# Kernel tuning notes

Hardware: AMD Instinct MI355X
Metric: run time of the kernel (lower is better)

## Reference

```python
import jax, jax.numpy as jnp
import numpy as np

N = 16384
HID = 256
MI = 128
POS_PER_NODE = 4
TEMP = 0.5


def setup_inputs() -> dict:
    key = jax.random.key(0)
    k1, k2, k3, k4 = jax.random.split(key, 4)
    h_v1 = jax.random.normal(k1, (N, HID), dtype=jnp.float32)
    h_v2 = jax.random.normal(k2, (N, HID), dtype=jnp.float32)
    W = jax.random.normal(k3, (HID, MI), dtype=jnp.float32) * (1.0 / np.sqrt(HID))
    b = jnp.zeros((MI,), dtype=jnp.float32)
    # 4 positives per row -> every row has a nonzero positive count
    pos_row = jnp.repeat(jnp.arange(N, dtype=jnp.int32), POS_PER_NODE)
    pos_col = jax.random.randint(k4, (N * POS_PER_NODE,), 0, N, dtype=jnp.int32)
    return {"h_v1": h_v1, "h_v2": h_v2, "W": W, "b": b,
            "pos_row": pos_row, "pos_col": pos_col}


def _l2norm(x):
    return x / jnp.linalg.norm(x, axis=-1, keepdims=True)


def _cal_loss_mi(e1, e2, pos_row, pos_col):
    # sim_mat[i,j] = <e1_i, e2_j> / T   (N x N, the big intermediate)
    sim = jnp.einsum('ik,jk->ij', e1, e2) / TEMP
    sim = sim - jax.lax.stop_gradient(jnp.max(sim, axis=1, keepdims=True))
    sim = jnp.exp(sim)
    sim_pos = sim[pos_row, pos_col]                      # [E] gather
    row_sum = jnp.sum(sim, axis=1)                       # [N]
    pos_sum = jax.ops.segment_sum(sim_pos, pos_row, num_segments=N)
    denom = (row_sum - pos_sum)[pos_row]                 # [E]
    log_lv = jnp.log(sim_pos / denom)                    # [E]
    pos_cnt = jax.ops.segment_sum(jnp.ones_like(sim_pos), pos_row, num_segments=N)
    per_row = jax.ops.segment_sum(log_lv, pos_row, num_segments=N) / pos_cnt
    return -jnp.mean(per_row)


def reference(h_v1, h_v2, W, b, pos_row, pos_col):
    p1 = _l2norm(jax.nn.relu(h_v1 @ W + b))
    p2 = _l2norm(jax.nn.relu(h_v2 @ W + b))
    loss = 0.5 * (_cal_loss_mi(p1, p2, pos_row, pos_col)
                  + _cal_loss_mi(p2, p1, pos_row, pos_col))
    return loss
```

## Files before the change

kernel.cpp:

```cpp
#include <hip/hip_runtime.h>

typedef unsigned short ushort_t;
typedef unsigned int uint32;
typedef __attribute__((ext_vector_type(8))) short short8;
typedef __attribute__((ext_vector_type(4))) float f32x4;
typedef __attribute__((ext_vector_type(2))) float f32x2;

#define HID 256
#define MI 128
#define ALPHA 2.8853900817779268f
#define LN2F 0.69314718055994531f

__device__ __forceinline__ float bflo(uint32 u) { return __uint_as_float(u << 16); }
__device__ __forceinline__ float bfhi(uint32 u) { return __uint_as_float(u & 0xffff0000u); }
__device__ __forceinline__ ushort_t f2bf(float f) {
  uint32 u = __float_as_uint(f);
  u += 0x7fffu + ((u >> 16) & 1u);
  return (ushort_t)(u >> 16);
}

__global__ __launch_bounds__(256) void proj_kernel(
    const float* __restrict__ h1, const float* __restrict__ h2,
    const float* __restrict__ W, const float* __restrict__ b,
    ushort_t* __restrict__ p1b, ushort_t* __restrict__ p2b,
    float* __restrict__ fbase, int nz, float* __restrict__ out, int n)
{
  __shared__ __align__(16) unsigned char wt[65536];
  int t = threadIdx.x;
  int lane = t & 63, w = t >> 6;
  int lr = lane & 15, lg = lane >> 4;
  long R0 = (long)blockIdx.x * 64;
  const float* src = (R0 < n) ? (h1 + R0 * HID) : (h2 + (R0 - n) * HID);
  ushort_t* dst = (R0 < n) ? (p1b + R0 * MI) : (p2b + (R0 - n) * MI);
  float scale = (R0 < n) ? ALPHA : 1.0f;

  {
    int base = blockIdx.x * 224;
    if (t < 224 && base + t < nz) fbase[base + t] = 0.f;
    if (blockIdx.x == 0 && t == 0) out[0] = 0.f;
  }

  #pragma unroll
  for (int i = 0; i < 32; ++i) {
    int idx4 = i * 1024 + t * 4;
    float4 v = *(const float4*)(W + idx4);
    int k = idx4 >> 7, nc0 = idx4 & 127;
    int g = k >> 3, klo = (k & 7) * 2;
    #pragma unroll
    for (int j = 0; j < 4; ++j) {
      int nc = nc0 + j;
      float f = (j == 0) ? v.x : (j == 1) ? v.y : (j == 2) ? v.z : v.w;
      *(ushort_t*)(wt + nc * 512 + ((g ^ (nc & 31)) << 4) + klo) = f2bf(f);
    }
  }

  float bb[8];
  #pragma unroll
  for (int ch = 0; ch < 8; ++ch) bb[ch] = b[ch * 16 + lr];

  int row = w * 16 + lr;
  const float* hrow = src + (size_t)row * HID;
  float4 v0[8], v1[8];
  #pragma unroll
  for (int kt = 0; kt < 8; ++kt) {
    v0[kt] = *(const float4*)(hrow + kt * 32 + lg * 8);
    v1[kt] = *(const float4*)(hrow + kt * 32 + lg * 8 + 4);
  }
  short8 afr[8];
  #pragma unroll
  for (int kt = 0; kt < 8; ++kt) {
    short8 a;
    a[0] = (short)f2bf(v0[kt].x); a[1] = (short)f2bf(v0[kt].y);
    a[2] = (short)f2bf(v0[kt].z); a[3] = (short)f2bf(v0[kt].w);
    a[4] = (short)f2bf(v1[kt].x); a[5] = (short)f2bf(v1[kt].y);
    a[6] = (short)f2bf(v1[kt].z); a[7] = (short)f2bf(v1[kt].w);
    afr[kt] = a;
  }

  __syncthreads();

  f32x4 acc[8];
  #pragma unroll
  for (int ch = 0; ch < 8; ++ch) acc[ch] = (f32x4){0.f, 0.f, 0.f, 0.f};
  #pragma unroll
  for (int ch = 0; ch < 8; ++ch) {
    int ncol = ch * 16 + lr;
    #pragma unroll
    for (int kt = 0; kt < 8; ++kt) {
      int g = kt * 4 + lg;
      short8 bf = *(const short8*)(wt + ncol * 512 + ((g ^ (ncol & 31)) << 4));
      acc[ch] = __builtin_amdgcn_mfma_f32_16x16x32_bf16(afr[kt], bf, acc[ch], 0, 0, 0);
    }
  }

  #pragma unroll
  for (int r = 0; r < 4; ++r) {
    float v[8];
    float ss = 0.f;
    #pragma unroll
    for (int ch = 0; ch < 8; ++ch) {
      v[ch] = fmaxf(acc[ch][r] + bb[ch], 0.f);
      ss += v[ch] * v[ch];
    }
    ss += __shfl_xor(ss, 1, 64);
    ss += __shfl_xor(ss, 2, 64);
    ss += __shfl_xor(ss, 4, 64);
    ss += __shfl_xor(ss, 8, 64);
    float rn = rsqrtf(ss) * scale;
    int orow = w * 16 + lg * 4 + r;
    #pragma unroll
    for (int ch = 0; ch < 8; ++ch)
      dst[(size_t)orow * MI + ch * 16 + lr] = f2bf(v[ch] * rn);
  }
}

__global__ __launch_bounds__(256, 2) void sim_kernel(
    const ushort_t* __restrict__ p1b, const ushort_t* __restrict__ p2b,
    float* __restrict__ rowsum, float* __restrict__ colsum,
    const int* __restrict__ pos_row, const int* __restrict__ pos_col,
    float* __restrict__ psum1, float* __restrict__ psum2,
    float* __restrict__ srow1, float* __restrict__ srow2,
    float* __restrict__ cntb, int E)
{
  __shared__ __align__(16) unsigned char ldsB[65536];
  __shared__ float colacc[1024];
  int t = threadIdx.x;
  int lane = t & 63, w = t >> 6;
  int lr = lane & 15, lg = lane >> 4;
  int rowbase = blockIdx.y * 256 + w * 64;
  int jbase = blockIdx.x * 1024;

  uint4 st0, st1, st2, st3;
  int gs = t & 15, r0 = t >> 4;
  int sw = (gs ^ (r0 & 15)) << 4;

  auto load_stage = [&](int jt) {
    int j0 = jbase + jt * 64;
    const ushort_t* base = p2b + (size_t)(j0 + r0) * MI + (gs << 3);
    st0 = *(const uint4*)(base);
    st1 = *(const uint4*)(base + 16 * MI);
    st2 = *(const uint4*)(base + 32 * MI);
    st3 = *(const uint4*)(base + 48 * MI);
  };
  auto write_stage = [&](int buf) {
    unsigned char* base = ldsB + buf * 16384 + r0 * 256 + sw;
    *(uint4*)(base)            = st0;
    *(uint4*)(base + 16 * 256) = st1;
    *(uint4*)(base + 32 * 256) = st2;
    *(uint4*)(base + 48 * 256) = st3;
  };

  load_stage(0);

  short8 afr[4][4];
  #pragma unroll
  for (int rt = 0; rt < 4; ++rt)
    #pragma unroll
    for (int kt = 0; kt < 4; ++kt)
      afr[rt][kt] = *(const short8*)(p1b + (size_t)(rowbase + rt * 16 + lr) * MI + kt * 32 + lg * 8);

  colacc[t] = 0.f;
  colacc[256 + t] = 0.f;
  colacc[512 + t] = 0.f;
  colacc[768 + t] = 0.f;

  f32x2 rs2[4][2];
  #pragma unroll
  for (int rt = 0; rt < 4; ++rt) {
    rs2[rt][0] = (f32x2){0.f, 0.f};
    rs2[rt][1] = (f32x2){0.f, 0.f};
  }

  write_stage(0);
  load_stage(1);
  write_stage(1);
  __syncthreads();

  auto compute_tile = [&](int jt, const unsigned char* B) {
    #pragma unroll
    for (int ch = 0; ch < 4; ++ch) {
      f32x4 acc[4];
      #pragma unroll
      for (int rt = 0; rt < 4; ++rt) acc[rt] = (f32x4){0.f, 0.f, 0.f, 0.f};
      #pragma unroll
      for (int kt = 0; kt < 4; ++kt) {
        int ncol = ch * 16 + lr;
        int g = kt * 4 + lg;
        short8 bf = *(const short8*)(B + ncol * 256 + ((g ^ (ncol & 15)) << 4));
        #pragma unroll
        for (int rt = 0; rt < 4; ++rt)
          acc[rt] = __builtin_amdgcn_mfma_f32_16x16x32_bf16(afr[rt][kt], bf, acc[rt], 0, 0, 0);
      }
      f32x2 cs2 = (f32x2){0.f, 0.f};
      #pragma unroll
      for (int rt = 0; rt < 4; ++rt) {
        f32x2 e01, e23;
        e01[0] = __builtin_amdgcn_exp2f(acc[rt][0]);
        e01[1] = __builtin_amdgcn_exp2f(acc[rt][1]);
        e23[0] = __builtin_amdgcn_exp2f(acc[rt][2]);
        e23[1] = __builtin_amdgcn_exp2f(acc[rt][3]);
        rs2[rt][0] += e01;
        rs2[rt][1] += e23;
        cs2 += e01;
        cs2 += e23;
      }
      float csum = cs2[0] + cs2[1];
      csum += __shfl_xor(csum, 16, 64);
      csum += __shfl_xor(csum, 32, 64);
      if (lg == 0) atomicAdd(&colacc[jt * 64 + ch * 16 + lr], csum);
    }
  };

  for (int it = 0; it < 8; ++it) {
    int t0 = 2 * it, t1 = 2 * it + 1;
    const unsigned char* B0 = ldsB + (t0 & 3) * 16384;
    const unsigned char* B1 = ldsB + (t1 & 3) * 16384;
    if (it < 7) load_stage(t0 + 2);
    compute_tile(t0, B0);
    if (it < 7) {
      write_stage((t0 + 2) & 3);
      load_stage(t0 + 3);
    }
    compute_tile(t1, B1);
    if (it < 7) write_stage((t0 + 3) & 3);
    __syncthreads();
  }

  #pragma unroll
  for (int rt = 0; rt < 4; ++rt)
    #pragma unroll
    for (int j = 0; j < 2; ++j)
      #pragma unroll
      for (int s = 0; s < 2; ++s) {
        float v = rs2[rt][j][s];
        v += __shfl_xor(v, 1, 64);
        v += __shfl_xor(v, 2, 64);
        v += __shfl_xor(v, 4, 64);
        v += __shfl_xor(v, 8, 64);
        if (lr == 0) atomicAdd(&rowsum[rowbase + rt * 16 + lg * 4 + j * 2 + s], v);
      }

  atomicAdd(&colsum[jbase + t], colacc[t]);
  atomicAdd(&colsum[jbase + 256 + t], colacc[256 + t]);
  atomicAdd(&colsum[jbase + 512 + t], colacc[512 + t]);
  atomicAdd(&colsum[jbase + 768 + t], colacc[768 + t]);

  {
    int eb = blockIdx.y * gridDim.x + blockIdx.x;
    int e = eb * 64 + (t >> 2), q = t & 3;
    if (e < E) {
      int r = pos_row[e], c = pos_col[e];
      const uint4* a1 = (const uint4*)(p1b + (size_t)r * MI) + q * 4;
      const uint4* b1 = (const uint4*)(p2b + (size_t)c * MI) + q * 4;
      const uint4* a2 = (const uint4*)(p1b + (size_t)c * MI) + q * 4;
      const uint4* b2 = (const uint4*)(p2b + (size_t)r * MI) + q * 4;
      float d1 = 0.f, d2 = 0.f;
      #pragma unroll
      for (int it = 0; it < 4; ++it) {
        uint4 x = a1[it], y = b1[it];
        d1 += bflo(x.x) * bflo(y.x) + bfhi(x.x) * bfhi(y.x);
        d1 += bflo(x.y) * bflo(y.y) + bfhi(x.y) * bfhi(y.y);
        d1 += bflo(x.z) * bflo(y.z) + bfhi(x.z) * bfhi(y.z);
        d1 += bflo(x.w) * bflo(y.w) + bfhi(x.w) * bfhi(y.w);
        uint4 u = a2[it], v = b2[it];
        d2 += bflo(u.x) * bflo(v.x) + bfhi(u.x) * bfhi(v.x);
        d2 += bflo(u.y) * bflo(v.y) + bfhi(u.y) * bfhi(v.y);
        d2 += bflo(u.z) * bflo(v.z) + bfhi(u.z) * bfhi(v.z);
        d2 += bflo(u.w) * bflo(v.w) + bfhi(u.w) * bfhi(v.w);
      }
      d1 += __shfl_xor(d1, 1, 64);
      d1 += __shfl_xor(d1, 2, 64);
      d2 += __shfl_xor(d2, 1, 64);
      d2 += __shfl_xor(d2, 2, 64);
      if (q == 0) {
        float e1 = __builtin_amdgcn_exp2f(d1);
        float e2 = __builtin_amdgcn_exp2f(d2);
        atomicAdd(&psum1[r], e1);
        atomicAdd(&srow1[r], d1 * LN2F);
        atomicAdd(&psum2[r], e2);
        atomicAdd(&srow2[r], d2 * LN2F);
        atomicAdd(&cntb[r], 1.0f);
      }
    }
  }
}

__global__ __launch_bounds__(256) void finalize_kernel(
    const float* __restrict__ rowsum, const float* __restrict__ colsum,
    const float* __restrict__ psum1, const float* __restrict__ psum2,
    const float* __restrict__ srow1, const float* __restrict__ srow2,
    const float* __restrict__ cntb, float* __restrict__ out, int n)
{
  __shared__ float sred[4];
  int r = blockIdx.x * 256 + threadIdx.x;
  float local = 0.f;
  if (r < n) {
    float inv = 1.0f / cntb[r];
    float d1 = rowsum[r] - psum1[r];
    float d2 = colsum[r] - psum2[r];
    local = srow1[r] * inv - __builtin_amdgcn_logf(d1) * LN2F
          + srow2[r] * inv - __builtin_amdgcn_logf(d2) * LN2F;
  }
  #pragma unroll
  for (int m = 1; m <= 32; m <<= 1) local += __shfl_xor(local, m, 64);
  int lane = threadIdx.x & 63, wv = threadIdx.x >> 6;
  if (lane == 0) sred[wv] = local;
  __syncthreads();
  if (threadIdx.x == 0) {
    float tot = sred[0] + sred[1] + sred[2] + sred[3];
    atomicAdd(out, -tot / (2.0f * n));
  }
}

extern "C" void kernel_launch(void* const* d_in, const int* in_sizes, int n_in,
                              void* d_out, int out_size, void* d_ws, size_t ws_size,
                              hipStream_t stream)
{
  const float* h1 = (const float*)d_in[0];
  const float* h2 = (const float*)d_in[1];
  const float* W  = (const float*)d_in[2];
  const float* b  = (const float*)d_in[3];
  const int* pos_row = (const int*)d_in[4];
  const int* pos_col = (const int*)d_in[5];
  int n = in_sizes[0] / HID;
  int E = in_sizes[4];
  float* out = (float*)d_out;

  char* ws = (char*)d_ws;
  ushort_t* p1b = (ushort_t*)ws;
  ushort_t* p2b = p1b + (size_t)n * MI;
  float* fbase  = (float*)(ws + (size_t)2 * n * MI * sizeof(ushort_t));
  float* rowsum = fbase;
  float* colsum = rowsum + n;
  float* psum1  = colsum + n;
  float* psum2  = psum1 + n;
  float* srow1  = psum2 + n;
  float* srow2  = srow1 + n;
  float* cntb   = srow2 + n;

  int nz = 7 * n;
  proj_kernel<<<2 * n / 64, 256, 0, stream>>>(h1, h2, W, b, p1b, p2b,
                                              fbase, nz, out, n);
  dim3 g2(n / 1024, n / 256);
  sim_kernel<<<g2, 256, 0, stream>>>(p1b, p2b, rowsum, colsum,
                                     pos_row, pos_col, psum1, psum2,
                                     srow1, srow2, cntb, E);
  finalize_kernel<<<(n + 255) / 256, 256, 0, stream>>>(rowsum, colsum, psum1, psum2,
                                                       srow1, srow2, cntb, out, n);
}
```

Baseline: 186.1 us.

## Compute similarity matrix with FP8 MFMA instead of BF16

The projection kernel now also writes FP8-quantized copies of the normalized embeddings. The sim kernel loads these FP8 operands into half-size LDS stages and uses the 16x16x32 fp8 MFMA in place of the bf16 one. This halves operand bandwidth and LDS traffic and may raise MFMA throughput. In exchange, FP8 precision on logits that are scaled by 1/T·log2e adds error to the exp sums, which could hurt loss accuracy. The BF16 copies are still written and passed to the kernel, likely for the positive-pair gather.

```diff
diff --git a/kernel.cpp b/kernel.cpp
--- a/kernel.cpp
+++ b/kernel.cpp
@@ -1,6 +1,7 @@
 #include <hip/hip_runtime.h>
 
 typedef unsigned short ushort_t;
+typedef unsigned char uchar_t;
 typedef unsigned int uint32;
 typedef __attribute__((ext_vector_type(8))) short short8;
 typedef __attribute__((ext_vector_type(4))) float f32x4;
@@ -23,6 +24,7 @@
     const float* __restrict__ h1, const float* __restrict__ h2,
     const float* __restrict__ W, const float* __restrict__ b,
     ushort_t* __restrict__ p1b, ushort_t* __restrict__ p2b,
+    uchar_t* __restrict__ p1f8, uchar_t* __restrict__ p2f8,
     float* __restrict__ fbase, int nz, float* __restrict__ out, int n)
 {
   __shared__ __align__(16) unsigned char wt[65536];
@@ -32,6 +34,7 @@
   long R0 = (long)blockIdx.x * 64;
   const float* src = (R0 < n) ? (h1 + R0 * HID) : (h2 + (R0 - n) * HID);
   ushort_t* dst = (R0 < n) ? (p1b + R0 * MI) : (p2b + (R0 - n) * MI);
+  uchar_t* dst8 = (R0 < n) ? (p1f8 + R0 * MI) : (p2f8 + (R0 - n) * MI);
   float scale = (R0 < n) ? ALPHA : 1.0f;
 
   {
@@ -108,13 +111,23 @@
     ss += __shfl_xor(ss, 8, 64);
     float rn = rsqrtf(ss) * scale;
     int orow = w * 16 + lg * 4 + r;
-    #pragma unroll
-    for (int ch = 0; ch < 8; ++ch)
-      dst[(size_t)orow * MI + ch * 16 + lr] = f2bf(v[ch] * rn);
+    float vf[8];
+    #pragma unroll
+    for (int ch = 0; ch < 8; ++ch) {
+      vf[ch] = v[ch] * rn;
+      dst[(size_t)orow * MI + ch * 16 + lr] = f2bf(vf[ch]);
+    }
+    #pragma unroll
+    for (int ch = 0; ch < 8; ch += 2) {
+      int pk = __builtin_amdgcn_cvt_pk_fp8_f32(vf[ch], vf[ch + 1], 0, false);
+      dst8[(size_t)orow * MI + ch * 16 + lr] = (uchar_t)(pk & 0xff);
+      dst8[(size_t)orow * MI + (ch + 1) * 16 + lr] = (uchar_t)((pk >> 8) & 0xff);
+    }
   }
 }
 
 __global__ __launch_bounds__(256, 2) void sim_kernel(
+    const uchar_t* __restrict__ p1f8, const uchar_t* __restrict__ p2f8,
     const ushort_t* __restrict__ p1b, const ushort_t* __restrict__ p2b,
     float* __restrict__ rowsum, float* __restrict__ colsum,
     const int* __restrict__ pos_row, const int* __restrict__ pos_col,
@@ -122,7 +135,7 @@
     float* __restrict__ srow1, float* __restrict__ srow2,
     float* __restrict__ cntb, int E)
 {
-  __shared__ __align__(16) unsigned char ldsB[65536];
+  __shared__ __align__(16) unsigned char ldsB[32768];
   __shared__ float colacc[1024];
   int t = threadIdx.x;
   int lane = t & 63, w = t >> 6;
@@ -130,34 +143,30 @@
   int rowbase = blockIdx.y * 256 + w * 64;
   int jbase = blockIdx.x * 1024;
 
-  uint4 st0, st1, st2, st3;
-  int gs = t & 15, r0 = t >> 4;
-  int sw = (gs ^ (r0 & 15)) << 4;
+  uint4 st0, st1;
+  int gs = t & 7, c0 = t >> 3;
+  int sw = (gs ^ (c0 & 7)) << 4;
 
   auto load_stage = [&](int jt) {
     int j0 = jbase + jt * 64;
-    const ushort_t* base = p2b + (size_t)(j0 + r0) * MI + (gs << 3);
+    const uchar_t* base = p2f8 + (size_t)(j0 + c0) * MI + (gs << 4);
     st0 = *(const uint4*)(base);
-    st1 = *(const uint4*)(base + 16 * MI);
-    st2 = *(const uint4*)(base + 32 * MI);
-    st3 = *(const uint4*)(base + 48 * MI);
+    st1 = *(const uint4*)(base + 32 * MI);
   };
   auto write_stage = [&](int buf) {
-    unsigned char* base = ldsB + buf * 16384 + r0 * 256 + sw;
+    unsigned char* base = ldsB + buf * 8192 + c0 * 128 + sw;
     *(uint4*)(base)            = st0;
-    *(uint4*)(base + 16 * 256) = st1;
-    *(uint4*)(base + 32 * 256) = st2;
-    *(uint4*)(base + 48 * 256) = st3;
+    *(uint4*)(base + 32 * 128) = st1;
   };
 
   load_stage(0);
 
-  short8 afr[4][4];
+  long afr8[4][4];
   #pragma unroll
   for (int rt = 0; rt < 4; ++rt)
     #pragma unroll
     for (int kt = 0; kt < 4; ++kt)
-      afr[rt][kt] = *(const short8*)(p1b + (size_t)(rowbase + rt * 16 + lr) * MI + kt * 32 + lg * 8);
+      afr8[rt][kt] = *(const long*)(p1f8 + (size_t)(rowbase + rt * 16 + lr) * MI + kt * 32 + lg * 8);
 
   colacc[t] = 0.f;
   colacc[256 + t] = 0.f;
@@ -186,10 +195,10 @@
       for (int kt = 0; kt < 4; ++kt) {
         int ncol = ch * 16 + lr;
         int g = kt * 4 + lg;
-        short8 bf = *(const short8*)(B + ncol * 256 + ((g ^ (ncol & 15)) << 4));
+        long bf8 = *(const long*)(B + ncol * 128 + (((g >> 1) ^ (ncol & 7)) << 4) + ((g & 1) << 3));
         #pragma unroll
         for (int rt = 0; rt < 4; ++rt)
-          acc[rt] = __builtin_amdgcn_mfma_f32_16x16x32_bf16(afr[rt][kt], bf, acc[rt], 0, 0, 0);
+          acc[rt] = __builtin_amdgcn_mfma_f32_16x16x32_fp8_fp8(afr8[rt][kt], bf8, acc[rt], 0, 0, 0);
       }
       f32x2 cs2 = (f32x2){0.f, 0.f};
       #pragma unroll
@@ -213,8 +222,8 @@
 
   for (int it = 0; it < 8; ++it) {
     int t0 = 2 * it, t1 = 2 * it + 1;
-    const unsigned char* B0 = ldsB + (t0 & 3) * 16384;
-    const unsigned char* B1 = ldsB + (t1 & 3) * 16384;
+    const unsigned char* B0 = ldsB + (t0 & 3) * 8192;
+    const unsigned char* B1 = ldsB + (t1 & 3) * 8192;
     if (it < 7) load_stage(t0 + 2);
     compute_tile(t0, B0);
     if (it < 7) {
@@ -337,12 +346,14 @@
   float* srow1  = psum2 + n;
   float* srow2  = srow1 + n;
   float* cntb   = srow2 + n;
+  uchar_t* p1f8 = (uchar_t*)(cntb + n);
+  uchar_t* p2f8 = p1f8 + (size_t)n * MI;
 
   int nz = 7 * n;
   proj_kernel<<<2 * n / 64, 256, 0, stream>>>(h1, h2, W, b, p1b, p2b,
-                                              fbase, nz, out, n);
+                                              p1f8, p2f8, fbase, nz, out, n);
   dim3 g2(n / 1024, n / 256);
-  sim_kernel<<<g2, 256, 0, stream>>>(p1b, p2b, rowsum, colsum,
+  sim_kernel<<<g2, 256, 0, stream>>>(p1f8, p2f8, p1b, p2b, rowsum, colsum,
                                      pos_row, pos_col, psum1, psum2,
                                      srow1, srow2, cntb, E);
   finalize_kernel<<<(n + 255) / 256, 256, 0, stream>>>(rowsum, colsum, psum1, psum2,
```

Result: faster. 179.9 us (median of 3 runs) (-3.3%).
